# Performance work log

Measured on AMD Instinct MI355X. Metric: run time of the kernel, lower is better.

Reference implementation:

```python
import jax, jax.numpy as jnp
import numpy as np

B, S, H, W, C = 16, 32, 84, 84, 4
HID, NH, L, A = 256, 4, 2, 18
HD = HID // NH
THETA = 10000.0
EPS = 1e-6


def _ln(x, s, b):
    m = jnp.mean(x, axis=-1, keepdims=True)
    v = jnp.mean(jnp.square(x - m), axis=-1, keepdims=True)
    return (x - m) / jnp.sqrt(v + EPS) * s + b


def _conv(x, w):
    return jax.lax.conv_general_dilated(x, w, (1, 1), 'SAME', dimension_numbers=('NHWC', 'HWIO', 'NHWC'))


def _rotate_half(x):
    xe = x[..., ::2]
    xo = x[..., 1::2]
    return jnp.stack((-xo, xe), axis=-1).reshape(x.shape)


def _rope(q, k):
    d = q.shape[-1]
    pos = jnp.arange(q.shape[-2], dtype=jnp.float32)
    inv_freq = 1.0 / jnp.asarray(THETA, jnp.float32) ** (jnp.arange(0, d, 2, dtype=jnp.float32) / d)
    ang = pos[:, None] * inv_freq[None, :]
    sin = jnp.repeat(jnp.sin(ang), 2, axis=-1)[None, None].astype(q.dtype)
    cos = jnp.repeat(jnp.cos(ang), 2, axis=-1)[None, None].astype(q.dtype)
    return q * cos + _rotate_half(q) * sin, k * cos + _rotate_half(k) * sin


def setup_inputs() -> dict:
    key = jax.random.key(0)
    ks = jax.random.split(key, 20)
    he = lambda k, shp, fan: jax.random.normal(k, shp, jnp.float32) * np.sqrt(2.0 / fan)
    return {
        'x': jax.random.normal(ks[0], (B, S, H, W, C), jnp.float32),
        'attention_padding': jnp.ones((B, S), jnp.bool_),
        'conv0_w': he(ks[1], (3, 3, C, 32), 3 * 3 * C),
        'conv0_b': jnp.zeros((32,), jnp.float32),
        'ln_c0_s': jnp.ones((32,), jnp.float32), 'ln_c0_b': jnp.zeros((32,), jnp.float32),
        'conv1_w': he(ks[2], (3, 3, 32, 64), 3 * 3 * 32),
        'conv1_b': jnp.zeros((64,), jnp.float32),
        'ln_c1_s': jnp.ones((64,), jnp.float32), 'ln_c1_b': jnp.zeros((64,), jnp.float32),
        'proj_w': he(ks[3], (64, HID), 64), 'proj_b': jnp.zeros((HID,), jnp.float32),
        'ln_p_s': jnp.ones((HID,), jnp.float32), 'ln_p_b': jnp.zeros((HID,), jnp.float32),
        'attn_qkv_w': he(ks[4], (L, HID, 3 * HID), HID),
        'attn_qkv_b': jnp.zeros((L, 3 * HID), jnp.float32),
        'attn_out_w': he(ks[5], (L, HID, HID), HID),
        'attn_out_b': jnp.zeros((L, HID), jnp.float32),
        'ln_a_s': jnp.ones((L, HID), jnp.float32), 'ln_a_b': jnp.zeros((L, HID), jnp.float32),
        'up_w': he(ks[6], (L, HID, 2 * HID), HID),
        'down_w': he(ks[7], (L, 2 * HID, HID), 2 * HID),
        'ln_m_s': jnp.ones((L, HID), jnp.float32), 'ln_m_b': jnp.zeros((L, HID), jnp.float32),
        'head_w': he(ks[8], (HID, A), HID), 'head_b': jnp.zeros((A,), jnp.float32),
    }


def reference(x, attention_padding, conv0_w, conv0_b, ln_c0_s, ln_c0_b, conv1_w, conv1_b,
              ln_c1_s, ln_c1_b, proj_w, proj_b, ln_p_s, ln_p_b, attn_qkv_w, attn_qkv_b,
              attn_out_w, attn_out_b, ln_a_s, ln_a_b, up_w, down_w, ln_m_s, ln_m_b,
              head_w, head_b):
    b, s = x.shape[:2]
    # CNN feature extractor over flattened (B*S) frames
    h = x.reshape(b * s, *x.shape[2:])
    h = jax.nn.relu(_ln(_conv(h, conv0_w) + conv0_b, ln_c0_s, ln_c0_b))
    h = jax.nn.relu(_ln(_conv(h, conv1_w) + conv1_b, ln_c1_s, ln_c1_b))
    h = jnp.mean(h, axis=(1, 2)).reshape(b, s, -1)  # (B,S,64)
    h = _ln(h @ proj_w + proj_b, ln_p_s, ln_p_b)    # (B,S,HID)
    pad = attention_padding
    causal = jnp.tril(jnp.ones((s, s), jnp.bool_))
    mask = pad[:, None, None, :] & causal[None, None]
    scale = jnp.asarray(HD, h.dtype) ** (-0.5)
    neg = jnp.asarray(-1e9, h.dtype)
    for i in range(L):
        r = h
        qkv = h @ attn_qkv_w[i] + attn_qkv_b[i]
        q, k, v = jnp.split(qkv, 3, axis=-1)
        sh = lambda t: t.reshape(b, s, NH, HD).transpose(0, 2, 1, 3)
        q, k, v = sh(q), sh(k), sh(v)
        q, k = _rope(q, k)
        logits = jnp.einsum('bhqd,bhkd->bhqk', q, k) * scale
        attn = jax.nn.softmax(jnp.where(mask, logits, neg), axis=-1)
        y = jnp.einsum('bhqk,bhkd->bhqd', attn, v).transpose(0, 2, 1, 3).reshape(b, s, HID)
        y = (y @ attn_out_w[i] + attn_out_b[i]) * pad[:, :, None].astype(h.dtype)
        h = _ln(y, ln_a_s[i], ln_a_b[i]) + r
        r = h
        u = jax.nn.relu(h @ up_w[i])
        h = _ln(u @ down_w[i], ln_m_s[i], ln_m_b[i]) + r
    return h @ head_w + head_b  # (B,S,action_dim)
```

## Files before the change

### kernel.cpp

```cpp
#include <hip/hip_runtime.h>
#include <hip/hip_bf16.h>

#define LN_EPS 1e-6f

typedef __attribute__((ext_vector_type(8))) short bf16x8;
typedef __attribute__((ext_vector_type(4))) float fx4;

struct U8 { union { bf16x8 v; uint2 p[2]; }; };

__device__ __forceinline__ unsigned short f2bf(float f) {
    union { __hip_bfloat16 b; unsigned short u; } cv;
    cv.b = __float2bfloat16(f);
    return cv.u;
}

__global__ void k_pad(const unsigned char* __restrict__ p, float* __restrict__ padf) {
    __shared__ int cnt;
    int t = threadIdx.x;
    if (t == 0) cnt = 0;
    __syncthreads();
    if (p[t]) atomicAdd(&cnt, 1);
    __syncthreads();
    float v;
    if (cnt > 256) v = p[t] ? 1.f : 0.f;
    else           v = ((const int*)p)[t] ? 1.f : 0.f;
    padf[t] = v;
}

__global__ void k_wprep(const float* __restrict__ w1, const float* __restrict__ w0,
                        unsigned short* __restrict__ wtb) {
    int idx = blockIdx.x * 256 + threadIdx.x;
    if (idx < 18432) {
        int j  = idx & 7;
        int kg = (idx >> 3) & 3;
        int co = (idx >> 5) & 63;
        int tp = idx >> 11;
        wtb[idx] = f2bf(w1[((size_t)tp * 32 + kg * 8 + j) * 64 + co]);
    } else {
        int r = idx - 18432;
        int ch = r >> 6, k = r & 63;
        float v = 0.f;
        if (k < 36) v = w0[(size_t)k * 32 + ch];
        wtb[idx] = f2bf(v);
    }
}

__global__ void k_wpack(const float* __restrict__ qkvw, const float* __restrict__ ow,
                        const float* __restrict__ upw, const float* __restrict__ dww,
                        const float* __restrict__ pw, const float* __restrict__ hw,
                        unsigned short* __restrict__ wpk)
{
    int idx = blockIdx.x * 256 + threadIdx.x;
    if (idx >= 1073152) return;
    float v;
    if (idx < 393216) {
        int l = idx / 196608, rm = idx % 196608, n = rm >> 8, k = rm & 255;
        v = qkvw[((size_t)l * 256 + k) * 768 + n];
    } else if (idx < 524288) {
        int r = idx - 393216, l = r >> 16, rm = r & 65535, n = rm >> 8, k = rm & 255;
        v = ow[((size_t)l * 256 + k) * 256 + n];
    } else if (idx < 786432) {
        int r = idx - 524288, l = r >> 17, rm = r & 131071, n = rm >> 8, k = rm & 255;
        v = upw[((size_t)l * 256 + k) * 512 + n];
    } else if (idx < 1048576) {
        int r = idx - 786432, l = r >> 17, rm = r & 131071, n = rm >> 9, k = rm & 511;
        v = dww[((size_t)l * 512 + k) * 256 + n];
    } else if (idx < 1064960) {
        int r = idx - 1048576, n = r >> 6, k = r & 63;
        v = pw[k * 256 + n];
    } else {
        int r = idx - 1064960, n = r >> 8, k = r & 255;
        v = (n < 18) ? hw[(size_t)k * 18 + n] : 0.f;
    }
    wpk[idx] = f2bf(v);
}

__global__ __launch_bounds__(256, 3) void k_conv1(
    const float* __restrict__ x, const unsigned short* __restrict__ wtb,
    const float* __restrict__ c0b, const float* __restrict__ l0s, const float* __restrict__ l0b,
    const float* __restrict__ bias, const float* __restrict__ lns, const float* __restrict__ lnb,
    float* __restrict__ pooled)
{
    __shared__ __align__(16) unsigned short At[4][5][86][8];
    __shared__ __align__(16) unsigned short xs[7][86][4];
    __shared__ __align__(16) float pool_w[4][64];
    const int tid = threadIdx.x;
    const int img = blockIdx.x / 28;
    const int rg  = blockIdx.x - img * 28;
    const int y0  = rg * 3;

    const int lane = tid & 63;
    const int wv = tid >> 6;
    const int lo = lane & 15;
    const int kg = lane >> 4;

    if (tid >= 64 && tid < 104) {
        int z = tid - 64;
        int zk = z / 10, rem = z - zk * 10, zr = rem >> 1, side = rem & 1;
        *reinterpret_cast<uint4*>(&At[zk][zr][side ? 85 : 0][0]) = (uint4){0, 0, 0, 0};
    }
    if (tid >= 104 && tid < 118) {
        int z = tid - 104, row = z >> 1, side = z & 1;
        *reinterpret_cast<uint2*>(&xs[row][side ? 85 : 0][0]) = (uint2){0, 0};
    }
    for (int i = tid; i < 588; i += 256) {
        int row = i / 84, c = i - row * 84;
        int gy = y0 - 2 + row;
        float4 v = (float4){0.f, 0.f, 0.f, 0.f};
        if (gy >= 0 && gy < 84)
            v = *reinterpret_cast<const float4*>(x + ((size_t)img * 7056 + gy * 84 + c) * 4);
        unsigned l32 = (unsigned)f2bf(v.x) | ((unsigned)f2bf(v.y) << 16);
        unsigned h32 = (unsigned)f2bf(v.z) | ((unsigned)f2bf(v.w) << 16);
        *reinterpret_cast<uint2*>(&xs[row][c + 1][0]) = (uint2){l32, h32};
    }
    __syncthreads();

    {
        const unsigned short* wc0 = wtb + 18432;
        bf16x8 W0[2], W1[2];
        #pragma unroll
        for (int m = 0; m < 2; ++m) {
            W0[m] = *reinterpret_cast<const bf16x8*>(wc0 + (m * 16 + lo) * 64 + kg * 8);
            W1[m] = *reinterpret_cast<const bf16x8*>(wc0 + (m * 16 + lo) * 64 + 32 + kg * 8);
        }
        float cb[2][4], sg[2][4], bg[2][4];
        #pragma unroll
        for (int m = 0; m < 2; ++m)
            #pragma unroll
            for (int r = 0; r < 4; ++r) {
                int c = m * 16 + kg * 4 + r;
                cb[m][r] = c0b[c]; sg[m][r] = l0s[c]; bg[m][r] = l0b[c];
            }
        const int t0 = 2 * kg, t1 = 2 * kg + 1;
        const int dy0 = t0 / 3, dx0 = t0 % 3, dy1 = t1 / 3, dx1 = t1 % 3;
        const unsigned short* xsb = &xs[0][0][0];

        for (int it = 0; it < 7; ++it) {
            int np = it * 4 + wv;
            if (np >= 27) break;
            int px = np * 16 + lo;
            int pxc = px < 420 ? px : 419;
            int r5 = pxc / 84, col = pxc - r5 * 84;
            U8 a0u, a1u;
            a0u.p[0] = *reinterpret_cast<const uint2*>(xsb + ((r5 + dy0) * 86 + col + dx0) * 4);
            a0u.p[1] = *reinterpret_cast<const uint2*>(xsb + ((r5 + dy1) * 86 + col + dx1) * 4);
            if (kg == 0)
                a1u.p[0] = *reinterpret_cast<const uint2*>(xsb + ((r5 + 2) * 86 + col + 2) * 4);
            else
                a1u.p[0] = (uint2){0, 0};
            a1u.p[1] = (uint2){0, 0};

            fx4 c2[2];
            c2[0] = (fx4){0.f, 0.f, 0.f, 0.f};
            c2[1] = (fx4){0.f, 0.f, 0.f, 0.f};
            c2[0] = __builtin_amdgcn_mfma_f32_16x16x32_bf16(W0[0], a0u.v, c2[0], 0, 0, 0);
            c2[0] = __builtin_amdgcn_mfma_f32_16x16x32_bf16(W1[0], a1u.v, c2[0], 0, 0, 0);
            c2[1] = __builtin_amdgcn_mfma_f32_16x16x32_bf16(W0[1], a0u.v, c2[1], 0, 0, 0);
            c2[1] = __builtin_amdgcn_mfma_f32_16x16x32_bf16(W1[1], a1u.v, c2[1], 0, 0, 0);

            float v[2][4], s = 0.f, q = 0.f;
            #pragma unroll
            for (int m = 0; m < 2; ++m)
                #pragma unroll
                for (int r = 0; r < 4; ++r) {
                    v[m][r] = c2[m][r] + cb[m][r];
                    s += v[m][r]; q += v[m][r] * v[m][r];
                }
            s += __shfl_xor(s, 16); q += __shfl_xor(q, 16);
            s += __shfl_xor(s, 32); q += __shfl_xor(q, 32);
            float mn = s * (1.f / 32.f);
            float inv = rsqrtf(q * (1.f / 32.f) - mn * mn + LN_EPS);

            if (px < 420) {
                int yA = y0 - 1 + r5;
                bool gv = (unsigned)yA < 84u;
                #pragma unroll
                for (int m = 0; m < 2; ++m) {
                    uint2 pk = (uint2){0, 0};
                    if (gv) {
                        unsigned short o0 = f2bf(fmaxf((v[m][0] - mn) * inv * sg[m][0] + bg[m][0], 0.f));
                        unsigned short o1 = f2bf(fmaxf((v[m][1] - mn) * inv * sg[m][1] + bg[m][1], 0.f));
                        unsigned short o2 = f2bf(fmaxf((v[m][2] - mn) * inv * sg[m][2] + bg[m][2], 0.f));
                        unsigned short o3 = f2bf(fmaxf((v[m][3] - mn) * inv * sg[m][3] + bg[m][3], 0.f));
                        pk.x = (unsigned)o0 | ((unsigned)o1 << 16);
                        pk.y = (unsigned)o2 | ((unsigned)o3 << 16);
                    }
                    *reinterpret_cast<uint2*>(&At[2 * m + (kg >> 1)][r5][col + 1][(kg & 1) * 4]) = pk;
                }
            }
        }
    }
    __syncthreads();

    int abase[4];
    #pragma unroll
    for (int n = 0; n < 4; ++n) {
        int pl = wv * 64 + n * 16 + lo;
        if (pl > 251) pl = 251;
        int rl = pl / 84;
        int c = pl - rl * 84;
        abase[n] = ((kg * 5 + rl) * 86 + c) * 8;
    }

    fx4 acc[4][4];
    #pragma unroll
    for (int m = 0; m < 4; ++m)
        #pragma unroll
        for (int n = 0; n < 4; ++n) acc[m][n] = (fx4){0.f, 0.f, 0.f, 0.f};

    const unsigned short* Abase = &At[0][0][0][0];
    #pragma unroll
    for (int dy = 0; dy < 3; ++dy) {
        #pragma unroll
        for (int dx = 0; dx < 3; ++dx) {
            const int t = dy * 3 + dx;
            bf16x8 Wf[4];
            #pragma unroll
            for (int m = 0; m < 4; ++m)
                Wf[m] = *reinterpret_cast<const bf16x8*>(
                    wtb + (size_t)((t * 64 + m * 16 + lo) * 4 + kg) * 8);
            #pragma unroll
            for (int n = 0; n < 4; ++n) {
                bf16x8 Pf = *reinterpret_cast<const bf16x8*>(Abase + abase[n] + (dy * 86 + dx) * 8);
                #pragma unroll
                for (int m = 0; m < 4; ++m)
                    acc[m][n] = __builtin_amdgcn_mfma_f32_16x16x32_bf16(Wf[m], Pf, acc[m][n], 0, 0, 0);
            }
        }
    }

    float s4[4] = {0.f, 0.f, 0.f, 0.f}, q4[4] = {0.f, 0.f, 0.f, 0.f};
    #pragma unroll
    for (int m = 0; m < 4; ++m) {
        float4 cbv = *reinterpret_cast<const float4*>(bias + m * 16 + kg * 4);
        #pragma unroll
        for (int n = 0; n < 4; ++n)
            #pragma unroll
            for (int r = 0; r < 4; ++r) {
                float val = acc[m][n][r] + (&cbv.x)[r];
                acc[m][n][r] = val;
                s4[n] += val; q4[n] += val * val;
            }
    }
    float mn4[4], iv4[4], pval[4];
    #pragma unroll
    for (int n = 0; n < 4; ++n) {
        float s = s4[n], q = q4[n];
        s += __shfl_xor(s, 16); q += __shfl_xor(q, 16);
        s += __shfl_xor(s, 32); q += __shfl_xor(q, 32);
        float mn = s * (1.f / 64.f);
        mn4[n] = mn;
        iv4[n] = rsqrtf(q * (1.f / 64.f) - mn * mn + LN_EPS);
        pval[n] = (wv * 64 + n * 16 + lo < 252) ? 1.f : 0.f;
    }
    float pool[4][4] = {{0.f}};
    #pragma unroll
    for (int m = 0; m < 4; ++m) {
        float4 sgv = *reinterpret_cast<const float4*>(lns + m * 16 + kg * 4);
        float4 bgv = *reinterpret_cast<const float4*>(lnb + m * 16 + kg * 4);
        #pragma unroll
        for (int n = 0; n < 4; ++n)
            #pragma unroll
            for (int r = 0; r < 4; ++r) {
                float o = fmaxf((acc[m][n][r] - mn4[n]) * iv4[n] * (&sgv.x)[r] + (&bgv.x)[r], 0.f);
                pool[m][r] = fmaf(o, pval[n], pool[m][r]);
            }
    }
    #pragma unroll
    for (int off = 1; off < 16; off <<= 1)
        #pragma unroll
        for (int m = 0; m < 4; ++m)
            #pragma unroll
            for (int r = 0; r < 4; ++r)
                pool[m][r] += __shfl_xor(pool[m][r], off);
    if (lo == 0) {
        #pragma unroll
        for (int m = 0; m < 4; ++m) {
            float4 pk = (float4){pool[m][0], pool[m][1], pool[m][2], pool[m][3]};
            *reinterpret_cast<float4*>(&pool_w[wv][m * 16 + kg * 4]) = pk;
        }
    }
    __syncthreads();
    if (tid < 64) {
        float s = pool_w[0][tid] + pool_w[1][tid] + pool_w[2][tid] + pool_w[3][tid];
        atomicAdd(&pooled[img * 64 + tid], s);
    }
}

template<int MT, int NT, int KS>
__device__ __forceinline__ void mfma_gemm(
    const unsigned short* A, int lda, int m0,
    const unsigned short* B, int ldb, int nt0,
    fx4 (&acc)[MT][NT], int lane)
{
    const int lo = lane & 15, kg = lane >> 4;
    #pragma unroll
    for (int ks = 0; ks < KS; ++ks) {
        const int k = ks * 32 + kg * 8;
        bf16x8 af[MT];
        #pragma unroll
        for (int m = 0; m < MT; ++m)
            af[m] = *reinterpret_cast<const bf16x8*>(A + (size_t)((m0 + m) * 16 + lo) * lda + k);
        #pragma unroll
        for (int n = 0; n < NT; ++n) {
            bf16x8 bf = *reinterpret_cast<const bf16x8*>(B + (size_t)((nt0 + n) * 16 + lo) * ldb + k);
            #pragma unroll
            for (int m = 0; m < MT; ++m)
                acc[m][n] = __builtin_amdgcn_mfma_f32_16x16x32_bf16(af[m], bf, acc[m][n], 0, 0, 0);
        }
    }
}

__device__ __forceinline__ void ln_update(
    const float* outs , float* hs, unsigned short* hs_b,
    const float* gs, const float* gb, bool resid, int w, int lane)
{
    #pragma unroll
    for (int i = 0; i < 4; ++i) {
        int r = w * 4 + i;
        float x[4], s = 0.f, q = 0.f;
        #pragma unroll
        for (int j = 0; j < 4; ++j) {
            x[j] = outs[r * 257 + lane + 64 * j];
            s += x[j]; q += x[j] * x[j];
        }
        #pragma unroll
        for (int off = 1; off < 64; off <<= 1) {
            s += __shfl_xor(s, off);
            q += __shfl_xor(q, off);
        }
        float mn = s * (1.f / 256.f);
        float inv = rsqrtf(q * (1.f / 256.f) - mn * mn + LN_EPS);
        #pragma unroll
        for (int j = 0; j < 4; ++j) {
            int c = lane + 64 * j;
            float nv = (x[j] - mn) * inv * gs[c] + gb[c];
            if (resid) nv += hs[r * 256 + c];
            hs[r * 256 + c] = nv;
            hs_b[r * 264 + c] = f2bf(nv);
        }
    }
}

__global__ __launch_bounds__(512) void k_xformer(
    const float* __restrict__ pooled, const float* __restrict__ padf,
    const unsigned short* __restrict__ wpk,
    const float* __restrict__ pb, const float* __restrict__ lps, const float* __restrict__ lpb,
    const float* __restrict__ qkvb, const float* __restrict__ obv,
    const float* __restrict__ las, const float* __restrict__ lab,
    const float* __restrict__ lms, const float* __restrict__ lmb,
    const float* __restrict__ hb, float* __restrict__ out)
{
    __shared__ __align__(16) char smem[124032];
    float* hs = (float*)(smem);
    unsigned short* hs_b = (unsigned short*)(smem + 32768);
    unsigned short* R1 = (unsigned short*)(smem + 49664);
    unsigned short* q_s = R1;
    unsigned short* k_s = R1 + 9216;
    unsigned short* us_b = R1;
    unsigned short* v_cm = (unsigned short*)(smem + 86528);
    unsigned short* ys_b = (unsigned short*)(smem + 107008);
    float* outs = (float*)(smem + 86528);
    unsigned short* pool_b = (unsigned short*)(smem + 86528);
    float* padc = (float*)(smem + 123904);

    const int b = blockIdx.x, t = threadIdx.x;
    const int w = t >> 6, lane = t & 63, lo = lane & 15, kg = lane >> 4;

    if (t < 32) padc[t] = padf[b * 32 + t];
    for (int i = t; i < 2048; i += 512) {
        int r = i >> 6, k = i & 63;
        pool_b[r * 72 + k] = f2bf(pooled[((size_t)b * 32 + r) * 64 + k] * (1.f / 7056.f));
    }
    __syncthreads();

    {
        fx4 acc[1][4];
        #pragma unroll
        for (int n = 0; n < 4; ++n) acc[0][n] = (fx4){0.f, 0.f, 0.f, 0.f};
        int m0 = w & 1, nt0 = (w >> 1) * 4;
        mfma_gemm<1, 4, 2>(pool_b, 72, m0, wpk + 1048576, 64, nt0, acc, lane);
        __syncthreads();
        #pragma unroll
        for (int n = 0; n < 4; ++n) {
            int c = (nt0 + n) * 16 + lo;
            float bias = pb[c];
            #pragma unroll
            for (int rg = 0; rg < 4; ++rg)
                outs[(m0 * 16 + kg * 4 + rg) * 257 + c] = acc[0][n][rg] + bias;
        }
        __syncthreads();
        ln_update(outs, hs, hs_b, lps, lpb, false, w, lane);
        __syncthreads();
    }

    for (int l = 0; l < 2; ++l) {
        const unsigned short* wq = wpk + (size_t)l * 196608;
        const unsigned short* wo = wpk + 393216 + (size_t)l * 65536;
        const unsigned short* wu = wpk + 524288 + (size_t)l * 131072;
        const unsigned short* wd = wpk + 786432 + (size_t)l * 131072;

        {
            fx4 acc[2][6];
            #pragma unroll
            for (int m = 0; m < 2; ++m)
                #pragma unroll
                for (int n = 0; n < 6; ++n) acc[m][n] = (fx4){0.f, 0.f, 0.f, 0.f};
            int nt0 = w * 6;
            mfma_gemm<2, 6, 8>(hs_b, 264, 0, wq, 256, nt0, acc, lane);
            #pragma unroll
            for (int n = 0; n < 6; ++n) {
                int c = (nt0 + n) * 16 + lo;
                int kind = c >> 8, cl = c & 255, h = cl >> 6, d = cl & 63;
                float bias = qkvb[l * 768 + c];
                if (kind < 2) {
                    int j = d >> 1;
                    float freq = exp2f(-(float)j * 0.41524101186f);
                    unsigned short* dst = (kind ? k_s : q_s) + h * 2304;
                    #pragma unroll
                    for (int m = 0; m < 2; ++m)
                        #pragma unroll
                        for (int rg = 0; rg < 4; ++rg) {
                            float val = acc[m][n][rg] + bias;
                            float prt = __shfl_xor(val, 1);
                            int r = m * 16 + kg * 4 + rg;
                            float sn, cs;
                            __sincosf((float)r * freq, &sn, &cs);
                            float rv = (d & 1) ? (val * cs + prt * sn) : (val * cs - prt * sn);
                            dst[r * 72 + d] = f2bf(rv);
                        }
                } else {
                    #pragma unroll
                    for (int m = 0; m < 2; ++m)
                        #pragma unroll
                        for (int rg = 0; rg < 4; ++rg) {
                            int r = m * 16 + kg * 4 + rg;
                            v_cm[(h * 64 + d) * 40 + r] = f2bf(acc[m][n][rg] + bias);
                        }
                }
            }
            __syncthreads();
        }

        {
            int h = w >> 1, mt = w & 1;
            fx4 sc[1][2];
            sc[0][0] = (fx4){0.f, 0.f, 0.f, 0.f};
            sc[0][1] = (fx4){0.f, 0.f, 0.f, 0.f};
            mfma_gemm<1, 2, 2>(q_s + h * 2304, 72, mt, k_s + h * 2304, 72, 0, sc, lane);
            __syncthreads();
            unsigned short* pa = R1 + h * 2304;
            float pad0 = padc[lo], pad1 = padc[16 + lo];
            #pragma unroll
            for (int rg = 0; rg < 4; ++rg) {
                int qr = mt * 16 + kg * 4 + rg;
                float v0 = (lo <= qr && pad0 != 0.f) ? sc[0][0][rg] * 0.125f : -1e9f;
                float v1 = ((16 + lo) <= qr && pad1 != 0.f) ? sc[0][1][rg] * 0.125f : -1e9f;
                float mx = fmaxf(v0, v1);
                #pragma unroll
                for (int off = 1; off < 16; off <<= 1) mx = fmaxf(mx, __shfl_xor(mx, off));
                float e0 = __expf(v0 - mx), e1 = __expf(v1 - mx);
                float sm = e0 + e1;
                #pragma unroll
                for (int off = 1; off < 16; off <<= 1) sm += __shfl_xor(sm, off);
                float inv = 1.f / sm;
                pa[qr * 40 + lo] = f2bf(e0 * inv);
                pa[qr * 40 + 16 + lo] = f2bf(e1 * inv);
            }
            __syncthreads();
        }

        {
            int h = w >> 1, mt = w & 1;
            fx4 yv[1][4];
            #pragma unroll
            for (int n = 0; n < 4; ++n) yv[0][n] = (fx4){0.f, 0.f, 0.f, 0.f};
            mfma_gemm<1, 4, 1>(R1 + h * 2304, 40, mt, v_cm + h * 2560, 40, 0, yv, lane);
            #pragma unroll
            for (int n = 0; n < 4; ++n) {
                int d = n * 16 + lo;
                #pragma unroll
                for (int rg = 0; rg < 4; ++rg)
                    ys_b[(mt * 16 + kg * 4 + rg) * 264 + h * 64 + d] = f2bf(yv[0][n][rg]);
            }
            __syncthreads();
        }

        {
            fx4 ac[2][2];
            #pragma unroll
            for (int m = 0; m < 2; ++m) { ac[m][0] = (fx4){0.f,0.f,0.f,0.f}; ac[m][1] = (fx4){0.f,0.f,0.f,0.f}; }
            mfma_gemm<2, 2, 8>(ys_b, 264, 0, wo, 256, w * 2, ac, lane);
            __syncthreads();
            #pragma unroll
            for (int n = 0; n < 2; ++n) {
                int c = (w * 2 + n) * 16 + lo;
                float bias = obv[l * 256 + c];
                #pragma unroll
                for (int m = 0; m < 2; ++m)
                    #pragma unroll
                    for (int rg = 0; rg < 4; ++rg) {
                        int r = m * 16 + kg * 4 + rg;
                        outs[r * 257 + c] = (ac[m][n][rg] + bias) * padc[r];
                    }
            }
            __syncthreads();
            ln_update(outs, hs, hs_b, las + l * 256, lab + l * 256, true, w, lane);
            __syncthreads();
        }

        {
            fx4 au[2][4];
            #pragma unroll
            for (int m = 0; m < 2; ++m)
                #pragma unroll
                for (int n = 0; n < 4; ++n) au[m][n] = (fx4){0.f, 0.f, 0.f, 0.f};
            mfma_gemm<2, 4, 8>(hs_b, 264, 0, wu, 256, w * 4, au, lane);
            #pragma unroll
            for (int n = 0; n < 4; ++n) {
                int c = (w * 4 + n) * 16 + lo;
                #pragma unroll
                for (int m = 0; m < 2; ++m)
                    #pragma unroll
                    for (int rg = 0; rg < 4; ++rg)
                        us_b[(m * 16 + kg * 4 + rg) * 520 + c] = f2bf(fmaxf(au[m][n][rg], 0.f));
            }
            __syncthreads();
        }

        {
            fx4 ad[2][2];
            #pragma unroll
            for (int m = 0; m < 2; ++m) { ad[m][0] = (fx4){0.f,0.f,0.f,0.f}; ad[m][1] = (fx4){0.f,0.f,0.f,0.f}; }
            mfma_gemm<2, 2, 16>(us_b, 520, 0, wd, 512, w * 2, ad, lane);
            #pragma unroll
            for (int n = 0; n < 2; ++n) {
                int c = (w * 2 + n) * 16 + lo;
                #pragma unroll
                for (int m = 0; m < 2; ++m)
                    #pragma unroll
                    for (int rg = 0; rg < 4; ++rg)
                        outs[(m * 16 + kg * 4 + rg) * 257 + c] = ad[m][n][rg];
            }
            __syncthreads();
            ln_update(outs, hs, hs_b, lms + l * 256, lmb + l * 256, true, w, lane);
            __syncthreads();
        }
    }

    if (w < 4) {
        int mt = w >> 1, nt = w & 1;
        fx4 hd[1][1];
        hd[0][0] = (fx4){0.f, 0.f, 0.f, 0.f};
        mfma_gemm<1, 1, 8>(hs_b, 264, mt, wpk + 1064960, 256, nt, hd, lane);
        int cc = nt * 16 + lo;
        if (cc < 18) {
            float bias = hb[cc];
            #pragma unroll
            for (int rg = 0; rg < 4; ++rg)
                out[((size_t)b * 32 + mt * 16 + kg * 4 + rg) * 18 + cc] = hd[0][0][rg] + bias;
        }
    }
}

extern "C" void kernel_launch(void* const* d_in, const int* in_sizes, int n_in,
                              void* d_out, int out_size, void* d_ws, size_t ws_size,
                              hipStream_t stream)
{
    (void)in_sizes; (void)n_in; (void)out_size; (void)ws_size;
    const float* x   = (const float*)d_in[0];
    const unsigned char* pad = (const unsigned char*)d_in[1];
    const float* c0w = (const float*)d_in[2];
    const float* c0b = (const float*)d_in[3];
    const float* l0s = (const float*)d_in[4];
    const float* l0b = (const float*)d_in[5];
    const float* c1w = (const float*)d_in[6];
    const float* c1b = (const float*)d_in[7];
    const float* l1s = (const float*)d_in[8];
    const float* l1b = (const float*)d_in[9];
    const float* pw  = (const float*)d_in[10];
    const float* pb  = (const float*)d_in[11];
    const float* lps = (const float*)d_in[12];
    const float* lpb = (const float*)d_in[13];
    const float* qkvw = (const float*)d_in[14];
    const float* qkvb = (const float*)d_in[15];
    const float* ow  = (const float*)d_in[16];
    const float* obv = (const float*)d_in[17];
    const float* las = (const float*)d_in[18];
    const float* lab = (const float*)d_in[19];
    const float* upw = (const float*)d_in[20];
    const float* dww = (const float*)d_in[21];
    const float* lms = (const float*)d_in[22];
    const float* lmb = (const float*)d_in[23];
    const float* hw  = (const float*)d_in[24];
    const float* hb  = (const float*)d_in[25];
    float* out = (float*)d_out;

    char* ws = (char*)d_ws;
    size_t off = 0;
    auto alloc = [&](size_t bytes) -> void* {
        void* p = ws + off;
        off = (off + bytes + 255) & ~(size_t)255;
        return p;
    };
    unsigned short* wtb = (unsigned short*)alloc(20480 * 2);
    unsigned short* wpk = (unsigned short*)alloc((size_t)1073152 * 2);
    float* pooled = (float*)alloc(512 * 64 * 4);
    float* padf   = (float*)alloc(512 * 4);

    hipMemsetAsync(pooled, 0, 512 * 64 * 4, stream);
    k_pad<<<1, 512, 0, stream>>>(pad, padf);
    k_wprep<<<80, 256, 0, stream>>>(c1w, c0w, wtb);
    k_wpack<<<4192, 256, 0, stream>>>(qkvw, ow, upw, dww, pw, hw, wpk);
    k_conv1<<<14336, 256, 0, stream>>>(x, wtb, c0b, l0s, l0b, c1b, l1s, l1b, pooled);
    k_xformer<<<16, 512, 0, stream>>>(pooled, padf, wpk, pb, lps, lpb,
                                      qkvb, obv, las, lab, lms, lmb, hb, out);
}
```

Baseline: 407.0 us.

## Process six output rows per conv block and double transformer threads

The fused conv kernel now handles 6 output rows per block instead of 3, so each block computes a 8-row intermediate conv0 tile. That cuts the halo recomputation of conv0 from 5/3 to 8/6 rows per output row and halves the block count, running the conv1 MFMA pass twice per block. Separately, the transformer kernel goes from 512 to 1024 threads, splitting each GEMM's N tiles across 16 waves and restricting attention scoring to the first 8 waves. The larger conv tile uses more LDS, which may lower occupancy under launch bounds of 3 blocks.

Result: slower. 678.7 us (+66.7%).

```diff
diff --git a/kernel.cpp b/kernel.cpp
--- a/kernel.cpp
+++ b/kernel.cpp
@@ -81,29 +81,29 @@
     const float* __restrict__ bias, const float* __restrict__ lns, const float* __restrict__ lnb,
     float* __restrict__ pooled)
 {
-    __shared__ __align__(16) unsigned short At[4][5][86][8];
-    __shared__ __align__(16) unsigned short xs[7][86][4];
+    __shared__ __align__(16) unsigned short At[4][8][86][8];
+    __shared__ __align__(16) unsigned short xs[10][86][4];
     __shared__ __align__(16) float pool_w[4][64];
     const int tid = threadIdx.x;
-    const int img = blockIdx.x / 28;
-    const int rg  = blockIdx.x - img * 28;
-    const int y0  = rg * 3;
+    const int img = blockIdx.x / 14;
+    const int rg  = blockIdx.x - img * 14;
+    const int y0  = rg * 6;
 
     const int lane = tid & 63;
     const int wv = tid >> 6;
     const int lo = lane & 15;
     const int kg = lane >> 4;
 
-    if (tid >= 64 && tid < 104) {
-        int z = tid - 64;
-        int zk = z / 10, rem = z - zk * 10, zr = rem >> 1, side = rem & 1;
+    if (tid >= 128 && tid < 192) {
+        int z = tid - 128;
+        int zk = z >> 4, rem = z & 15, zr = rem >> 1, side = rem & 1;
         *reinterpret_cast<uint4*>(&At[zk][zr][side ? 85 : 0][0]) = (uint4){0, 0, 0, 0};
     }
-    if (tid >= 104 && tid < 118) {
+    if (tid >= 104 && tid < 124) {
         int z = tid - 104, row = z >> 1, side = z & 1;
         *reinterpret_cast<uint2*>(&xs[row][side ? 85 : 0][0]) = (uint2){0, 0};
     }
-    for (int i = tid; i < 588; i += 256) {
+    for (int i = tid; i < 840; i += 256) {
         int row = i / 84, c = i - row * 84;
         int gy = y0 - 2 + row;
         float4 v = (float4){0.f, 0.f, 0.f, 0.f};
@@ -135,12 +135,11 @@
         const int dy0 = t0 / 3, dx0 = t0 % 3, dy1 = t1 / 3, dx1 = t1 % 3;
         const unsigned short* xsb = &xs[0][0][0];
 
-        for (int it = 0; it < 7; ++it) {
-            int np = it * 4 + wv;
-            if (np >= 27) break;
-            int px = np * 16 + lo;
-            int pxc = px < 420 ? px : 419;
-            int r5 = pxc / 84, col = pxc - r5 * 84;
+        for (int it = 0; it < 11; ++it) {
+            int tb = it * 4 + wv;
+            if (tb >= 42) break;
+            int px = tb * 16 + lo;
+            int r5 = px / 84, col = px - r5 * 84;
             U8 a0u, a1u;
             a0u.p[0] = *reinterpret_cast<const uint2*>(xsb + ((r5 + dy0) * 86 + col + dx0) * 4);
             a0u.p[1] = *reinterpret_cast<const uint2*>(xsb + ((r5 + dy1) * 86 + col + dx1) * 4);
@@ -171,100 +170,101 @@
             float mn = s * (1.f / 32.f);
             float inv = rsqrtf(q * (1.f / 32.f) - mn * mn + LN_EPS);
 
-            if (px < 420) {
-                int yA = y0 - 1 + r5;
-                bool gv = (unsigned)yA < 84u;
-                #pragma unroll
-                for (int m = 0; m < 2; ++m) {
-                    uint2 pk = (uint2){0, 0};
-                    if (gv) {
-                        unsigned short o0 = f2bf(fmaxf((v[m][0] - mn) * inv * sg[m][0] + bg[m][0], 0.f));
-                        unsigned short o1 = f2bf(fmaxf((v[m][1] - mn) * inv * sg[m][1] + bg[m][1], 0.f));
-                        unsigned short o2 = f2bf(fmaxf((v[m][2] - mn) * inv * sg[m][2] + bg[m][2], 0.f));
-                        unsigned short o3 = f2bf(fmaxf((v[m][3] - mn) * inv * sg[m][3] + bg[m][3], 0.f));
-                        pk.x = (unsigned)o0 | ((unsigned)o1 << 16);
-                        pk.y = (unsigned)o2 | ((unsigned)o3 << 16);
-                    }
-                    *reinterpret_cast<uint2*>(&At[2 * m + (kg >> 1)][r5][col + 1][(kg & 1) * 4]) = pk;
+            int yA = y0 - 1 + r5;
+            bool gv = (unsigned)yA < 84u;
+            #pragma unroll
+            for (int m = 0; m < 2; ++m) {
+                uint2 pk = (uint2){0, 0};
+                if (gv) {
+                    unsigned short o0 = f2bf(fmaxf((v[m][0] - mn) * inv * sg[m][0] + bg[m][0], 0.f));
+                    unsigned short o1 = f2bf(fmaxf((v[m][1] - mn) * inv * sg[m][1] + bg[m][1], 0.f));
+                    unsigned short o2 = f2bf(fmaxf((v[m][2] - mn) * inv * sg[m][2] + bg[m][2], 0.f));
+                    unsigned short o3 = f2bf(fmaxf((v[m][3] - mn) * inv * sg[m][3] + bg[m][3], 0.f));
+                    pk.x = (unsigned)o0 | ((unsigned)o1 << 16);
+                    pk.y = (unsigned)o2 | ((unsigned)o3 << 16);
                 }
+                *reinterpret_cast<uint2*>(&At[2 * m + (kg >> 1)][r5][col + 1][(kg & 1) * 4]) = pk;
             }
         }
     }
     __syncthreads();
 
-    int abase[4];
-    #pragma unroll
-    for (int n = 0; n < 4; ++n) {
-        int pl = wv * 64 + n * 16 + lo;
-        if (pl > 251) pl = 251;
-        int rl = pl / 84;
-        int c = pl - rl * 84;
-        abase[n] = ((kg * 5 + rl) * 86 + c) * 8;
-    }
-
-    fx4 acc[4][4];
-    #pragma unroll
-    for (int m = 0; m < 4; ++m)
-        #pragma unroll
-        for (int n = 0; n < 4; ++n) acc[m][n] = (fx4){0.f, 0.f, 0.f, 0.f};
-
+    float pool[4][4] = {{0.f}};
     const unsigned short* Abase = &At[0][0][0][0];
-    #pragma unroll
-    for (int dy = 0; dy < 3; ++dy) {
-        #pragma unroll
-        for (int dx = 0; dx < 3; ++dx) {
-            const int t = dy * 3 + dx;
-            bf16x8 Wf[4];
-            #pragma unroll
-            for (int m = 0; m < 4; ++m)
-                Wf[m] = *reinterpret_cast<const bf16x8*>(
-                    wtb + (size_t)((t * 64 + m * 16 + lo) * 4 + kg) * 8);
-            #pragma unroll
-            for (int n = 0; n < 4; ++n) {
-                bf16x8 Pf = *reinterpret_cast<const bf16x8*>(Abase + abase[n] + (dy * 86 + dx) * 8);
+    for (int p = 0; p < 2; ++p) {
+        const int pbase = p * 256;
+        int abase[4];
+        #pragma unroll
+        for (int n = 0; n < 4; ++n) {
+            int pl = pbase + wv * 64 + n * 16 + lo;
+            if (pl > 503) pl = 503;
+            int rl = pl / 84;
+            int c = pl - rl * 84;
+            abase[n] = ((kg * 8 + rl) * 86 + c) * 8;
+        }
+
+        fx4 acc[4][4];
+        #pragma unroll
+        for (int m = 0; m < 4; ++m)
+            #pragma unroll
+            for (int n = 0; n < 4; ++n) acc[m][n] = (fx4){0.f, 0.f, 0.f, 0.f};
+
+        #pragma unroll
+        for (int dy = 0; dy < 3; ++dy) {
+            #pragma unroll
+            for (int dx = 0; dx < 3; ++dx) {
+                const int t = dy * 3 + dx;
+                bf16x8 Wf[4];
                 #pragma unroll
                 for (int m = 0; m < 4; ++m)
-                    acc[m][n] = __builtin_amdgcn_mfma_f32_16x16x32_bf16(Wf[m], Pf, acc[m][n], 0, 0, 0);
-            }
-        }
-    }
-
-    float s4[4] = {0.f, 0.f, 0.f, 0.f}, q4[4] = {0.f, 0.f, 0.f, 0.f};
-    #pragma unroll
-    for (int m = 0; m < 4; ++m) {
-        float4 cbv = *reinterpret_cast<const float4*>(bias + m * 16 + kg * 4);
-        #pragma unroll
-        for (int n = 0; n < 4; ++n)
-            #pragma unroll
-            for (int r = 0; r < 4; ++r) {
-                float val = acc[m][n][r] + (&cbv.x)[r];
-                acc[m][n][r] = val;
-                s4[n] += val; q4[n] += val * val;
-            }
-    }
-    float mn4[4], iv4[4], pval[4];
-    #pragma unroll
-    for (int n = 0; n < 4; ++n) {
-        float s = s4[n], q = q4[n];
-        s += __shfl_xor(s, 16); q += __shfl_xor(q, 16);
-        s += __shfl_xor(s, 32); q += __shfl_xor(q, 32);
-        float mn = s * (1.f / 64.f);
-        mn4[n] = mn;
-        iv4[n] = rsqrtf(q * (1.f / 64.f) - mn * mn + LN_EPS);
-        pval[n] = (wv * 64 + n * 16 + lo < 252) ? 1.f : 0.f;
-    }
-    float pool[4][4] = {{0.f}};
-    #pragma unroll
-    for (int m = 0; m < 4; ++m) {
-        float4 sgv = *reinterpret_cast<const float4*>(lns + m * 16 + kg * 4);
-        float4 bgv = *reinterpret_cast<const float4*>(lnb + m * 16 + kg * 4);
-        #pragma unroll
-        for (int n = 0; n < 4; ++n)
-            #pragma unroll
-            for (int r = 0; r < 4; ++r) {
-                float o = fmaxf((acc[m][n][r] - mn4[n]) * iv4[n] * (&sgv.x)[r] + (&bgv.x)[r], 0.f);
-                pool[m][r] = fmaf(o, pval[n], pool[m][r]);
-            }
+                    Wf[m] = *reinterpret_cast<const bf16x8*>(
+                        wtb + (size_t)((t * 64 + m * 16 + lo) * 4 + kg) * 8);
+                #pragma unroll
+                for (int n = 0; n < 4; ++n) {
+                    bf16x8 Pf = *reinterpret_cast<const bf16x8*>(Abase + abase[n] + (dy * 86 + dx) * 8);
+                    #pragma unroll
+                    for (int m = 0; m < 4; ++m)
+                        acc[m][n] = __builtin_amdgcn_mfma_f32_16x16x32_bf16(Wf[m], Pf, acc[m][n], 0, 0, 0);
+                }
+            }
+        }
+
+        float s4[4] = {0.f, 0.f, 0.f, 0.f}, q4[4] = {0.f, 0.f, 0.f, 0.f};
+        #pragma unroll
+        for (int m = 0; m < 4; ++m) {
+            float4 cbv = *reinterpret_cast<const float4*>(bias + m * 16 + kg * 4);
+            #pragma unroll
+            for (int n = 0; n < 4; ++n)
+                #pragma unroll
+                for (int r = 0; r < 4; ++r) {
+                    float val = acc[m][n][r] + (&cbv.x)[r];
+                    acc[m][n][r] = val;
+                    s4[n] += val; q4[n] += val * val;
+                }
+        }
+        float mn4[4], iv4[4], pval[4];
+        #pragma unroll
+        for (int n = 0; n < 4; ++n) {
+            float s = s4[n], q = q4[n];
+            s += __shfl_xor(s, 16); q += __shfl_xor(q, 16);
+            s += __shfl_xor(s, 32); q += __shfl_xor(q, 32);
+            float mn = s * (1.f / 64.f);
+            mn4[n] = mn;
+            iv4[n] = rsqrtf(q * (1.f / 64.f) - mn * mn + LN_EPS);
+            pval[n] = (pbase + wv * 64 + n * 16 + lo < 504) ? 1.f : 0.f;
+        }
+        #pragma unroll
+        for (int m = 0; m < 4; ++m) {
+            float4 sgv = *reinterpret_cast<const float4*>(lns + m * 16 + kg * 4);
+            float4 bgv = *reinterpret_cast<const float4*>(lnb + m * 16 + kg * 4);
+            #pragma unroll
+            for (int n = 0; n < 4; ++n)
+                #pragma unroll
+                for (int r = 0; r < 4; ++r) {
+                    float o = fmaxf((acc[m][n][r] - mn4[n]) * iv4[n] * (&sgv.x)[r] + (&bgv.x)[r], 0.f);
+                    pool[m][r] = fmaf(o, pval[n], pool[m][r]);
+                }
+        }
     }
     #pragma unroll
     for (int off = 1; off < 16; off <<= 1)
@@ -316,8 +316,8 @@
     const float* gs, const float* gb, bool resid, int w, int lane)
 {
     #pragma unroll
-    for (int i = 0; i < 4; ++i) {
-        int r = w * 4 + i;
+    for (int i = 0; i < 2; ++i) {
+        int r = w * 2 + i;
         float x[4], s = 0.f, q = 0.f;
         #pragma unroll
         for (int j = 0; j < 4; ++j) {
@@ -342,7 +342,7 @@
     }
 }
 
-__global__ __launch_bounds__(512) void k_xformer(
+__global__ __launch_bounds__(1024) void k_xformer(
     const float* __restrict__ pooled, const float* __restrict__ padf,
     const unsigned short* __restrict__ wpk,
     const float* __restrict__ pb, const float* __restrict__ lps, const float* __restrict__ lpb,
@@ -368,21 +368,21 @@
     const int w = t >> 6, lane = t & 63, lo = lane & 15, kg = lane >> 4;
 
     if (t < 32) padc[t] = padf[b * 32 + t];
-    for (int i = t; i < 2048; i += 512) {
+    for (int i = t; i < 2048; i += 1024) {
         int r = i >> 6, k = i & 63;
         pool_b[r * 72 + k] = f2bf(pooled[((size_t)b * 32 + r) * 64 + k] * (1.f / 7056.f));
     }
     __syncthreads();
 
     {
-        fx4 acc[1][4];
-        #pragma unroll
-        for (int n = 0; n < 4; ++n) acc[0][n] = (fx4){0.f, 0.f, 0.f, 0.f};
-        int m0 = w & 1, nt0 = (w >> 1) * 4;
-        mfma_gemm<1, 4, 2>(pool_b, 72, m0, wpk + 1048576, 64, nt0, acc, lane);
+        fx4 acc[1][2];
+        acc[0][0] = (fx4){0.f, 0.f, 0.f, 0.f};
+        acc[0][1] = (fx4){0.f, 0.f, 0.f, 0.f};
+        int m0 = w & 1, nt0 = (w >> 1) * 2;
+        mfma_gemm<1, 2, 2>(pool_b, 72, m0, wpk + 1048576, 64, nt0, acc, lane);
         __syncthreads();
         #pragma unroll
-        for (int n = 0; n < 4; ++n) {
+        for (int n = 0; n < 2; ++n) {
             int c = (nt0 + n) * 16 + lo;
             float bias = pb[c];
             #pragma unroll
@@ -401,15 +401,15 @@
         const unsigned short* wd = wpk + 786432 + (size_t)l * 131072;
 
         {
-            fx4 acc[2][6];
+            fx4 acc[2][3];
             #pragma unroll
             for (int m = 0; m < 2; ++m)
                 #pragma unroll
-                for (int n = 0; n < 6; ++n) acc[m][n] = (fx4){0.f, 0.f, 0.f, 0.f};
-            int nt0 = w * 6;
-            mfma_gemm<2, 6, 8>(hs_b, 264, 0, wq, 256, nt0, acc, lane);
-            #pragma unroll
-            for (int n = 0; n < 6; ++n) {
+                for (int n = 0; n < 3; ++n) acc[m][n] = (fx4){0.f, 0.f, 0.f, 0.f};
+            int nt0 = w * 3;
+            mfma_gemm<2, 3, 8>(hs_b, 264, 0, wq, 256, nt0, acc, lane);
+            #pragma unroll
+            for (int n = 0; n < 3; ++n) {
                 int c = (nt0 + n) * 16 + lo;
                 int kind = c >> 8, cl = c & 255, h = cl >> 6, d = cl & 63;
                 float bias = qkvb[l * 768 + c];
@@ -443,42 +443,45 @@
         }
 
         {
-            int h = w >> 1, mt = w & 1;
             fx4 sc[1][2];
             sc[0][0] = (fx4){0.f, 0.f, 0.f, 0.f};
             sc[0][1] = (fx4){0.f, 0.f, 0.f, 0.f};
-            mfma_gemm<1, 2, 2>(q_s + h * 2304, 72, mt, k_s + h * 2304, 72, 0, sc, lane);
-            __syncthreads();
-            unsigned short* pa = R1 + h * 2304;
-            float pad0 = padc[lo], pad1 = padc[16 + lo];
-            #pragma unroll
-            for (int rg = 0; rg < 4; ++rg) {
-                int qr = mt * 16 + kg * 4 + rg;
-                float v0 = (lo <= qr && pad0 != 0.f) ? sc[0][0][rg] * 0.125f : -1e9f;
-                float v1 = ((16 + lo) <= qr && pad1 != 0.f) ? sc[0][1][rg] * 0.125f : -1e9f;
-                float mx = fmaxf(v0, v1);
-                #pragma unroll
-                for (int off = 1; off < 16; off <<= 1) mx = fmaxf(mx, __shfl_xor(mx, off));
-                float e0 = __expf(v0 - mx), e1 = __expf(v1 - mx);
-                float sm = e0 + e1;
-                #pragma unroll
-                for (int off = 1; off < 16; off <<= 1) sm += __shfl_xor(sm, off);
-                float inv = 1.f / sm;
-                pa[qr * 40 + lo] = f2bf(e0 * inv);
-                pa[qr * 40 + 16 + lo] = f2bf(e1 * inv);
+            int h = w >> 1, mt = w & 1;
+            if (w < 8)
+                mfma_gemm<1, 2, 2>(q_s + h * 2304, 72, mt, k_s + h * 2304, 72, 0, sc, lane);
+            __syncthreads();
+            if (w < 8) {
+                unsigned short* pa = R1 + h * 2304;
+                float pad0 = padc[lo], pad1 = padc[16 + lo];
+                #pragma unroll
+                for (int rg = 0; rg < 4; ++rg) {
+                    int qr = mt * 16 + kg * 4 + rg;
+                    float v0 = (lo <= qr && pad0 != 0.f) ? sc[0][0][rg] * 0.125f : -1e9f;
+                    float v1 = ((16 + lo) <= qr && pad1 != 0.f) ? sc[0][1][rg] * 0.125f : -1e9f;
+                    float mx = fmaxf(v0, v1);
+                    #pragma unroll
+                    for (int off = 1; off < 16; off <<= 1) mx = fmaxf(mx, __shfl_xor(mx, off));
+                    float e0 = __expf(v0 - mx), e1 = __expf(v1 - mx);
+                    float sm = e0 + e1;
+                    #pragma unroll
+                    for (int off = 1; off < 16; off <<= 1) sm += __shfl_xor(sm, off);
+                    float inv = 1.f / sm;
+                    pa[qr * 40 + lo] = f2bf(e0 * inv);
+                    pa[qr * 40 + 16 + lo] = f2bf(e1 * inv);
+                }
             }
             __syncthreads();
         }
 
         {
-            int h = w >> 1, mt = w & 1;
-            fx4 yv[1][4];
-            #pragma unroll
-            for (int n = 0; n < 4; ++n) yv[0][n] = (fx4){0.f, 0.f, 0.f, 0.f};
-            mfma_gemm<1, 4, 1>(R1 + h * 2304, 40, mt, v_cm + h * 2560, 40, 0, yv, lane);
-            #pragma unroll
-            for (int n = 0; n < 4; ++n) {
-                int d = n * 16 + lo;
+            int h = w >> 2, mt = (w >> 1) & 1, nh = w & 1;
+            fx4 yv[1][2];
+            yv[0][0] = (fx4){0.f, 0.f, 0.f, 0.f};
+            yv[0][1] = (fx4){0.f, 0.f, 0.f, 0.f};
+            mfma_gemm<1, 2, 1>(R1 + h * 2304, 40, mt, v_cm + h * 2560, 40, nh * 2, yv, lane);
+            #pragma unroll
+            for (int n = 0; n < 2; ++n) {
+                int d = (nh * 2 + n) * 16 + lo;
                 #pragma unroll
                 for (int rg = 0; rg < 4; ++rg)
                     ys_b[(mt * 16 + kg * 4 + rg) * 264 + h * 64 + d] = f2bf(yv[0][n][rg]);
@@ -487,21 +490,20 @@
         }
 
         {
-            fx4 ac[2][2];
-            #pragma unroll
-            for (int m = 0; m < 2; ++m) { ac[m][0] = (fx4){0.f,0.f,0.f,0.f}; ac[m][1] = (fx4){0.f,0.f,0.f,0.f}; }
-            mfma_gemm<2, 2, 8>(ys_b, 264, 0, wo, 256, w * 2, ac, lane);
-            __syncthreads();
-            #pragma unroll
-            for (int n = 0; n < 2; ++n) {
-                int c = (w * 2 + n) * 16 + lo;
+            fx4 ac[2][1];
+            ac[0][0] = (fx4){0.f, 0.f, 0.f, 0.f};
+            ac[1][0] = (fx4){0.f, 0.f, 0.f, 0.f};
+            mfma_gemm<2, 1, 8>(ys_b, 264, 0, wo, 256, w, ac, lane);
+            __syncthreads();
+            {
+                int c = w * 16 + lo;
                 float bias = obv[l * 256 + c];
                 #pragma unroll
                 for (int m = 0; m < 2; ++m)
                     #pragma unroll
                     for (int rg = 0; rg < 4; ++rg) {
                         int r = m * 16 + kg * 4 + rg;
-                        outs[r * 257 + c] = (ac[m][n][rg] + bias) * padc[r];
+                        outs[r * 257 + c] = (ac[m][0][rg] + bias) * padc[r];
                     }
             }
             __syncthreads();
@@ -510,15 +512,14 @@
         }
 
         {
-            fx4 au[2][4];
-            #pragma unroll
-            for (int m = 0; m < 2; ++m)
-                #pragma unroll
-                for (int n = 0; n < 4; ++n) au[m][n] = (fx4){0.f, 0.f, 0.f, 0.f};
-            mfma_gemm<2, 4, 8>(hs_b, 264, 0, wu, 256, w * 4, au, lane);
-            #pragma unroll
-            for (int n = 0; n < 4; ++n) {
-                int c = (w * 4 + n) * 16 + lo;
+            fx4 au[2][2];
+            #pragma unroll
+            for (int m = 0; m < 2; ++m) { au[m][0] = (fx4){0.f,0.f,0.f,0.f}; au[m][1] = (fx4){0.f,0.f,0.f,0.f}; }
+            int nt0 = w * 2;
+            mfma_gemm<2, 2, 8>(hs_b, 264, 0, wu, 256, nt0, au, lane);
+            #pragma unroll
+            for (int n = 0; n < 2; ++n) {
+                int c = (nt0 + n) * 16 + lo;
                 #pragma unroll
                 for (int m = 0; m < 2; ++m)
                     #pragma unroll
@@ -529,18 +530,17 @@
         }
 
         {
-            fx4 ad[2][2];
-            #pragma unroll
-            for (int m = 0; m < 2; ++m) { ad[m][0] = (fx4){0.f,0.f,0.f,0.f}; ad[m][1] = (fx4){0.f,0.f,0.f,0.f}; }
-            mfma_gemm<2, 2, 16>(us_b, 520, 0, wd, 512, w * 2, ad, lane);
-            #pragma unroll
-            for (int n = 0; n < 2; ++n) {
-                int c = (w * 2 + n) * 16 + lo;
+            fx4 ad[2][1];
+            ad[0][0] = (fx4){0.f, 0.f, 0.f, 0.f};
+            ad[1][0] = (fx4){0.f, 0.f, 0.f, 0.f};
+            mfma_gemm<2, 1, 16>(us_b, 520, 0, wd, 512, w, ad, lane);
+            {
+                int c = w * 16 + lo;
                 #pragma unroll
                 for (int m = 0; m < 2; ++m)
                     #pragma unroll
                     for (int rg = 0; rg < 4; ++rg)
-                        outs[(m * 16 + kg * 4 + rg) * 257 + c] = ad[m][n][rg];
+                        outs[(m * 16 + kg * 4 + rg) * 257 + c] = ad[m][0][rg];
             }
             __syncthreads();
             ln_update(outs, hs, hs_b, lms + l * 256, lmb + l * 256, true, w, lane);
@@ -612,7 +612,7 @@
     k_pad<<<1, 512, 0, stream>>>(pad, padf);
     k_wprep<<<80, 256, 0, stream>>>(c1w, c0w, wtb);
     k_wpack<<<4192, 256, 0, stream>>>(qkvw, ow, upw, dww, pw, hw, wpk);
-    k_conv1<<<14336, 256, 0, stream>>>(x, wtb, c0b, l0s, l0b, c1b, l1s, l1b, pooled);
-    k_xformer<<<16, 512, 0, stream>>>(pooled, padf, wpk, pb, lps, lpb,
-                                      qkvb, obv, las, lab, lms, lmb, hb, out);
-}
+    k_conv1<<<7168, 256, 0, stream>>>(x, wtb, c0b, l0s, l0b, c1b, l1s, l1b, pooled);
+    k_xformer<<<16, 1024, 0, stream>>>(pooled, padf, wpk, pb, lps, lpb,
+                                       qkvb, obv, las, lab, lms, lmb, hb, out);
+}
```
